# Kernel optimization log

Measured on AMD Instinct MI355X. Metric: run time of the kernel, lower is better.

## Reference

```python
import jax, jax.numpy as jnp
import numpy as np

N = 500000  # n_nodes; note module requires n_edges == n_nodes for final broadcast
E = 500000
IN_F = 128
OUT_F = 128


def setup_inputs() -> dict:
    key = jax.random.key(0)
    k1, k2, k3, k4 = jax.random.split(key, 4)
    x = jax.random.normal(k1, (N, IN_F), dtype=jnp.float32)
    edge_index = jax.random.randint(k2, (2, E), 0, N, dtype=jnp.int64)
    # xavier_uniform-ish scale for weight and att
    w_bound = float(np.sqrt(6.0 / (IN_F + OUT_F)))
    weight = jax.random.uniform(k3, (IN_F, OUT_F), jnp.float32, -w_bound, w_bound)
    a_bound = float(np.sqrt(6.0 / (1 + 2 * OUT_F)))
    att = jax.random.uniform(k4, (1, 2 * OUT_F), jnp.float32, -a_bound, a_bound)
    bias = jnp.zeros((OUT_F,), dtype=jnp.float32)
    return {"x": x, "edge_index": edge_index, "weight": weight, "att": att, "bias": bias}


def reference(x, edge_index, weight, att, bias):
    # Linear transform: [N, in] @ [in, out] -> [N, out]
    h = jnp.matmul(x, weight)
    row, col = edge_index[0], edge_index[1]
    # scatter-add aggregation: out[row] += h[col]
    out = jnp.zeros_like(h).at[row].add(h[col])
    out = jax.nn.relu(out + bias)
    # edge scores: (cat([out[row], out[col]]) * att).sum(-1)
    # expressed without materializing the [E, 2F] concat:
    a_src = att[0, :OUT_F]   # [F]
    a_dst = att[0, OUT_F:]   # [F]
    alpha = out[row] @ a_src + out[col] @ a_dst  # [E]
    alpha = jax.nn.leaky_relu(alpha, negative_slope=0.2)
    alpha = jax.nn.softmax(alpha, axis=0)  # global softmax over all edges
    # NOTE: original code broadcasts node-level out [N,F] against edge-level
    # alpha [E,1]; only valid because E == N, replicated faithfully here.
    return out * alpha[:, None]
```

## Files before the change

### kernel.cpp

```cpp
#include <hip/hip_runtime.h>

#define NN 500000
#define NE 500000
#define EPB 128

typedef _Float16 half8 __attribute__((ext_vector_type(8)));
typedef float floatx4 __attribute__((ext_vector_type(4)));

__device__ __align__(16) ushort g_wtf[4 * 8 * 64 * 8];
__device__ float    g_ssrc[NN];
__device__ float    g_sdst[NN];
__device__ float    g_alpha[NE];
__device__ unsigned g_maxenc;
__device__ float    g_denom;

__global__ __launch_bounds__(256) void k_zero(float4* __restrict__ p) {
  p[(size_t)blockIdx.x * 256 + threadIdx.x] = make_float4(0.f, 0.f, 0.f, 0.f);
}

__global__ __launch_bounds__(256) void k_prep_w(const float* __restrict__ w) {
  int idx = blockIdx.x * 256 + threadIdx.x;
  if (idx == 0) { g_maxenc = 0u; g_denom = 0.f; }
  int t = idx & 7;
  int fragidx = idx >> 3;
  int lane = fragidx & 63;
  int n = (fragidx >> 6) & 7;
  int kk = fragidx >> 9;
  int j = n * 16 + (lane & 15);
  int k = kk * 32 + (lane >> 4) * 8 + t;
  union { _Float16 h; ushort u; } cv;
  cv.h = (_Float16)w[k * 128 + j];
  g_wtf[idx] = cv.u;
}

__global__ __launch_bounds__(256, 4) void k_gemm_scatter(
    const float* __restrict__ x, const int* __restrict__ ei,
    float* __restrict__ out) {
  __shared__ __align__(16) ushort Ah[EPB * 128];
  __shared__ int rowids[EPB];
  __shared__ int colids[EPB];

  const int tid = threadIdx.x;
  const int base = blockIdx.x * EPB;

  if (tid < EPB) {
    int e = base + tid;
    int re = -1, ce = 0;
    if (e < NE) { re = ei[e]; ce = ei[NE + e]; }
    rowids[tid] = re;
    colids[tid] = ce;
  }
  __syncthreads();

  {
    const float4* x4 = (const float4*)x;
#pragma unroll
    for (int it = 0; it < (EPB * 32) / 256; ++it) {
      int i = tid + it * 256;
      int e = i >> 5, seg = i & 31;
      int cn = colids[e];
      float4 v = x4[cn * 32 + seg];
      union { _Float16 h[4]; uint2 u; } p;
      p.h[0] = (_Float16)v.x; p.h[1] = (_Float16)v.y;
      p.h[2] = (_Float16)v.z; p.h[3] = (_Float16)v.w;
      int hidx = (seg * 4) ^ ((e & 7) << 3);
      *(uint2*)&Ah[e * 128 + hidx] = p.u;
    }
  }
  __syncthreads();

  const int wid = tid >> 6;
  const int lane = tid & 63;
  const int l15 = lane & 15;
  const int lg = lane >> 4;
  const int ebase = wid * 32;
  const half8* __restrict__ wtf = (const half8*)g_wtf;

  floatx4 acc[2][8] = {};
#pragma unroll
  for (int kk = 0; kk < 4; ++kk) {
    const int k0 = kk * 32 + lg * 8;
    half8 a[2], b[8];
#pragma unroll
    for (int n = 0; n < 8; ++n) b[n] = wtf[(kk * 8 + n) * 64 + lane];
#pragma unroll
    for (int m = 0; m < 2; ++m) {
      int e = ebase + m * 16 + l15;
      a[m] = *(const half8*)&Ah[e * 128 + (k0 ^ ((e & 7) << 3))];
    }
#pragma unroll
    for (int n = 0; n < 8; ++n)
#pragma unroll
      for (int m = 0; m < 2; ++m)
        acc[m][n] = __builtin_amdgcn_mfma_f32_16x16x32_f16(a[m], b[n], acc[m][n], 0, 0, 0);
  }

#pragma unroll
  for (int m = 0; m < 2; ++m) {
#pragma unroll
    for (int r = 0; r < 4; ++r) {
      int el = ebase + m * 16 + lg * 4 + r;
      int rn = rowids[el];
      if (rn >= 0) {
        float* orow = out + (size_t)rn * 128;
#pragma unroll
        for (int n = 0; n < 8; ++n)
          unsafeAtomicAdd(&orow[n * 16 + l15], acc[m][n][r]);
      }
    }
  }
}

__global__ __launch_bounds__(256) void k_rowdots(
    const float* __restrict__ out, const float* __restrict__ att,
    const float* __restrict__ bias) {
  int tid = threadIdx.x;
  int lane32 = tid & 31;
  int row = blockIdx.x * 8 + (tid >> 5);
  const float4* o4 = (const float4*)out;
  const float4* b4 = (const float4*)bias;
  const float4* as4 = (const float4*)att;
  const float4* ad4 = (const float4*)(att + 128);
  float4 v = o4[(size_t)row * 32 + lane32];
  float4 bb = b4[lane32];
  v.x = fmaxf(v.x + bb.x, 0.f); v.y = fmaxf(v.y + bb.y, 0.f);
  v.z = fmaxf(v.z + bb.z, 0.f); v.w = fmaxf(v.w + bb.w, 0.f);
  float4 as = as4[lane32], ad = ad4[lane32];
  float ps = v.x * as.x + v.y * as.y + v.z * as.z + v.w * as.w;
  float pd = v.x * ad.x + v.y * ad.y + v.z * ad.z + v.w * ad.w;
#pragma unroll
  for (int off = 16; off; off >>= 1) {
    ps += __shfl_xor(ps, off);
    pd += __shfl_xor(pd, off);
  }
  if (lane32 == 0) { g_ssrc[row] = ps; g_sdst[row] = pd; }
}

__device__ __forceinline__ unsigned enc_f32(float x) {
  unsigned u = __float_as_uint(x);
  return (u & 0x80000000u) ? ~u : (u | 0x80000000u);
}

__global__ __launch_bounds__(256) void k_alpha_max(const int* __restrict__ ei) {
  int e = blockIdx.x * 256 + threadIdx.x;
  float a = -3.4e38f;
  if (e < NE) {
    int r = ei[e], c = ei[NE + e];
    float v = g_ssrc[r] + g_sdst[c];
    a = v > 0.f ? v : 0.2f * v;
    g_alpha[e] = a;
  }
#pragma unroll
  for (int off = 32; off; off >>= 1) a = fmaxf(a, __shfl_xor(a, off));
  __shared__ float wm[4];
  if ((threadIdx.x & 63) == 0) wm[threadIdx.x >> 6] = a;
  __syncthreads();
  if (threadIdx.x == 0) {
    float m = fmaxf(fmaxf(wm[0], wm[1]), fmaxf(wm[2], wm[3]));
    atomicMax(&g_maxenc, enc_f32(m));
  }
}

__global__ __launch_bounds__(256) void k_exp_sum() {
  unsigned encv = g_maxenc;
  unsigned u = (encv & 0x80000000u) ? (encv & 0x7fffffffu) : ~encv;
  float mx = __uint_as_float(u);
  int e = blockIdx.x * 256 + threadIdx.x;
  float v = 0.f;
  if (e < NE) {
    v = expf(g_alpha[e] - mx);
    g_alpha[e] = v;
  }
#pragma unroll
  for (int off = 32; off; off >>= 1) v += __shfl_xor(v, off);
  __shared__ float wsum[4];
  if ((threadIdx.x & 63) == 0) wsum[threadIdx.x >> 6] = v;
  __syncthreads();
  if (threadIdx.x == 0) atomicAdd(&g_denom, wsum[0] + wsum[1] + wsum[2] + wsum[3]);
}

__global__ __launch_bounds__(256) void k_scale(
    float* __restrict__ out, const float* __restrict__ bias) {
  int idx = blockIdx.x * 256 + threadIdx.x;
  int row = idx >> 5;
  float sc = g_alpha[row] / g_denom;
  float4* o4 = (float4*)out;
  const float4* b4 = (const float4*)bias;
  float4 bb = b4[idx & 31];
  float4 v = o4[idx];
  v.x = fmaxf(v.x + bb.x, 0.f) * sc;
  v.y = fmaxf(v.y + bb.y, 0.f) * sc;
  v.z = fmaxf(v.z + bb.z, 0.f) * sc;
  v.w = fmaxf(v.w + bb.w, 0.f) * sc;
  o4[idx] = v;
}

extern "C" void kernel_launch(void* const* d_in, const int* in_sizes, int n_in,
                              void* d_out, int out_size, void* d_ws, size_t ws_size,
                              hipStream_t stream) {
  const float* x    = (const float*)d_in[0];
  const int*   ei   = (const int*)d_in[1];
  const float* w    = (const float*)d_in[2];
  const float* att  = (const float*)d_in[3];
  const float* bias = (const float*)d_in[4];
  float* out = (float*)d_out;
  (void)d_ws; (void)ws_size; (void)in_sizes; (void)n_in; (void)out_size;

  k_zero<<<62500, 256, 0, stream>>>((float4*)out);
  k_prep_w<<<64, 256, 0, stream>>>(w);
  k_gemm_scatter<<<(NE + EPB - 1) / EPB, 256, 0, stream>>>(x, ei, out);
  k_rowdots<<<NN / 8, 256, 0, stream>>>(out, att, bias);
  k_alpha_max<<<(NE + 255) / 256, 256, 0, stream>>>(ei);
  k_exp_sum<<<(NE + 255) / 256, 256, 0, stream>>>();
  k_scale<<<NN * 32 / 256, 256, 0, stream>>>(out, bias);
}
```

Measured before the change: 759.3 us.

## Accumulate scatter-add in fp16 buffer using packed f16 atomics

Replaces the fp32 atomic scatter into the output with packed-half atomic adds into a separate fp16 global accumulator, pairing adjacent lanes via shuffle so each atomic carries two values. The downstream rowdot and scale kernels read the fp16 buffer, and zeroing covers half the bytes. This halves the atomic count and the memory traffic of the accumulate/read passes, at the cost of fp16 accumulation precision.

```diff
diff --git a/kernel.cpp b/kernel.cpp
--- a/kernel.cpp
+++ b/kernel.cpp
@@ -1,4 +1,5 @@
 #include <hip/hip_runtime.h>
+#include <hip/hip_fp16.h>
 
 #define NN 500000
 #define NE 500000
@@ -8,14 +9,16 @@
 typedef float floatx4 __attribute__((ext_vector_type(4)));
 
 __device__ __align__(16) ushort g_wtf[4 * 8 * 64 * 8];
+__device__ __align__(16) __half g_hacc[(size_t)NN * 128];
 __device__ float    g_ssrc[NN];
 __device__ float    g_sdst[NN];
 __device__ float    g_alpha[NE];
 __device__ unsigned g_maxenc;
 __device__ float    g_denom;
 
-__global__ __launch_bounds__(256) void k_zero(float4* __restrict__ p) {
-  p[(size_t)blockIdx.x * 256 + threadIdx.x] = make_float4(0.f, 0.f, 0.f, 0.f);
+__global__ __launch_bounds__(256) void k_zero(void) {
+  uint4* p = (uint4*)g_hacc;
+  p[(size_t)blockIdx.x * 256 + threadIdx.x] = make_uint4(0u, 0u, 0u, 0u);
 }
 
 __global__ __launch_bounds__(256) void k_prep_w(const float* __restrict__ w) {
@@ -34,8 +37,7 @@
 }
 
 __global__ __launch_bounds__(256, 4) void k_gemm_scatter(
-    const float* __restrict__ x, const int* __restrict__ ei,
-    float* __restrict__ out) {
+    const float* __restrict__ x, const int* __restrict__ ei) {
   __shared__ __align__(16) ushort Ah[EPB * 128];
   __shared__ int rowids[EPB];
   __shared__ int colids[EPB];
@@ -95,36 +97,47 @@
         acc[m][n] = __builtin_amdgcn_mfma_f32_16x16x32_f16(a[m], b[n], acc[m][n], 0, 0, 0);
   }
 
+  const bool evenlane = (lane & 1) == 0;
 #pragma unroll
   for (int m = 0; m < 2; ++m) {
 #pragma unroll
     for (int r = 0; r < 4; ++r) {
       int el = ebase + m * 16 + lg * 4 + r;
       int rn = rowids[el];
-      if (rn >= 0) {
-        float* orow = out + (size_t)rn * 128;
-#pragma unroll
-        for (int n = 0; n < 8; ++n)
-          unsafeAtomicAdd(&orow[n * 16 + l15], acc[m][n][r]);
+      __half* hrow = g_hacc + (size_t)(rn < 0 ? 0 : rn) * 128;
+#pragma unroll
+      for (int n = 0; n < 8; ++n) {
+        float v = acc[m][n][r];
+        float t = __shfl_xor(v, 1);
+        if (rn >= 0 && evenlane) {
+          union { _Float16 h[2]; unsigned u; } pk;
+          pk.h[0] = (_Float16)v;
+          pk.h[1] = (_Float16)t;
+          const __half* addr = &hrow[n * 16 + l15];
+          asm volatile("global_atomic_pk_add_f16 %0, %1, off"
+                       :: "v"(addr), "v"(pk.u) : "memory");
+        }
       }
     }
   }
+  asm volatile("s_waitcnt vmcnt(0)");
 }
 
 __global__ __launch_bounds__(256) void k_rowdots(
-    const float* __restrict__ out, const float* __restrict__ att,
-    const float* __restrict__ bias) {
+    const float* __restrict__ att, const float* __restrict__ bias) {
   int tid = threadIdx.x;
   int lane32 = tid & 31;
   int row = blockIdx.x * 8 + (tid >> 5);
-  const float4* o4 = (const float4*)out;
+  const __half2* h2 = (const __half2*)(g_hacc + (size_t)row * 128);
   const float4* b4 = (const float4*)bias;
   const float4* as4 = (const float4*)att;
   const float4* ad4 = (const float4*)(att + 128);
-  float4 v = o4[(size_t)row * 32 + lane32];
+  __half2 p0 = h2[lane32 * 2], p1 = h2[lane32 * 2 + 1];
+  float2 f0 = __half22float2(p0), f1 = __half22float2(p1);
   float4 bb = b4[lane32];
-  v.x = fmaxf(v.x + bb.x, 0.f); v.y = fmaxf(v.y + bb.y, 0.f);
-  v.z = fmaxf(v.z + bb.z, 0.f); v.w = fmaxf(v.w + bb.w, 0.f);
+  float4 v;
+  v.x = fmaxf(f0.x + bb.x, 0.f); v.y = fmaxf(f0.y + bb.y, 0.f);
+  v.z = fmaxf(f1.x + bb.z, 0.f); v.w = fmaxf(f1.y + bb.w, 0.f);
   float4 as = as4[lane32], ad = ad4[lane32];
   float ps = v.x * as.x + v.y * as.y + v.z * as.z + v.w * as.w;
   float pd = v.x * ad.x + v.y * ad.y + v.z * ad.z + v.w * ad.w;
@@ -182,17 +195,19 @@
 __global__ __launch_bounds__(256) void k_scale(
     float* __restrict__ out, const float* __restrict__ bias) {
   int idx = blockIdx.x * 256 + threadIdx.x;
-  int row = idx >> 5;
+  int row = idx >> 5, seg = idx & 31;
   float sc = g_alpha[row] / g_denom;
-  float4* o4 = (float4*)out;
+  const __half2* h2 = (const __half2*)(g_hacc + (size_t)row * 128);
+  __half2 p0 = h2[seg * 2], p1 = h2[seg * 2 + 1];
+  float2 f0 = __half22float2(p0), f1 = __half22float2(p1);
   const float4* b4 = (const float4*)bias;
-  float4 bb = b4[idx & 31];
-  float4 v = o4[idx];
-  v.x = fmaxf(v.x + bb.x, 0.f) * sc;
-  v.y = fmaxf(v.y + bb.y, 0.f) * sc;
-  v.z = fmaxf(v.z + bb.z, 0.f) * sc;
-  v.w = fmaxf(v.w + bb.w, 0.f) * sc;
-  o4[idx] = v;
+  float4 bb = b4[seg];
+  float4 v;
+  v.x = fmaxf(f0.x + bb.x, 0.f) * sc;
+  v.y = fmaxf(f0.y + bb.y, 0.f) * sc;
+  v.z = fmaxf(f1.x + bb.z, 0.f) * sc;
+  v.w = fmaxf(f1.y + bb.w, 0.f) * sc;
+  ((float4*)out)[idx] = v;
 }
 
 extern "C" void kernel_launch(void* const* d_in, const int* in_sizes, int n_in,
@@ -206,10 +221,10 @@
   float* out = (float*)d_out;
   (void)d_ws; (void)ws_size; (void)in_sizes; (void)n_in; (void)out_size;
 
-  k_zero<<<62500, 256, 0, stream>>>((float4*)out);
+  k_zero<<<31250, 256, 0, stream>>>();
   k_prep_w<<<64, 256, 0, stream>>>(w);
-  k_gemm_scatter<<<(NE + EPB - 1) / EPB, 256, 0, stream>>>(x, ei, out);
-  k_rowdots<<<NN / 8, 256, 0, stream>>>(out, att, bias);
+  k_gemm_scatter<<<(NE + EPB - 1) / EPB, 256, 0, stream>>>(x, ei);
+  k_rowdots<<<NN / 8, 256, 0, stream>>>(att, bias);
   k_alpha_max<<<(NE + 255) / 256, 256, 0, stream>>>(ei);
   k_exp_sum<<<(NE + 255) / 256, 256, 0, stream>>>();
   k_scale<<<NN * 32 / 256, 256, 0, stream>>>(out, bias);
```

New measurement: 835.1 us. +10.0%, slower.
